# Kernel optimization log

Measured on AMD Instinct MI355X. Metric: run time of the kernel, lower is better.

The kernel has to match this reference:

```python
import jax, jax.numpy as jnp
import numpy as np

B, C, H, W = 128, 512, 14, 14
HEADS = 4
DH = C // HEADS  # 128
RH = RW = 7      # reduced KV grid (hardcoded 7x7 in source)
EPS = 1e-5
SCALE = DH ** -0.5


def _rel_pos_index():
    # replicates RelativePositionBias.__init__ index construction (h=w=7)
    coords = np.stack(np.meshgrid(np.arange(RH), np.arange(RW), indexing='ij'))
    cf = coords.reshape(2, -1)                       # [2,49]
    rc = cf[:, :, None] - cf[:, None, :]             # [2,49,49]
    rc = rc.transpose(1, 2, 0).copy()                # [49,49,2]
    rc[:, :, 0] += RH - 1
    rc[:, :, 1] += RW - 1
    rc[:, :, 0] *= 2 * RH - 1
    return rc.sum(-1)                                # [49,49] int

REL_IDX = _rel_pos_index()


def batchnorm(x, g, b, m, v):
    inv = g / jnp.sqrt(v + EPS)
    return x * inv[None, :, None, None] + (b - m * inv)[None, :, None, None]


def dsconv(x, w_dw, w_pw):
    # depthwise 3x3 (pad 1, groups=C) then pointwise 1x1, no bias
    cin = x.shape[1]
    y = jax.lax.conv_general_dilated(
        x, w_dw, window_strides=(1, 1), padding=((1, 1), (1, 1)),
        dimension_numbers=('NCHW', 'OIHW', 'NCHW'), feature_group_count=cin)
    return jnp.einsum('bchw,oc->bohw', y, w_pw)


def bilinear_to_7(x):
    # F.interpolate(size=(7,7), mode='bilinear', align_corners=True)
    hin, win = x.shape[2], x.shape[3]
    ys = jnp.linspace(0.0, hin - 1, RH)
    xs = jnp.linspace(0.0, win - 1, RW)
    y0 = jnp.floor(ys).astype(jnp.int32); y1 = jnp.minimum(y0 + 1, hin - 1)
    x0 = jnp.floor(xs).astype(jnp.int32); x1 = jnp.minimum(x0 + 1, win - 1)
    wy = (ys - y0)[:, None]                          # [7,1]
    wx = (xs - x0)[None, :]                          # [1,7]
    v00 = x[:, :, y0][:, :, :, x0]; v01 = x[:, :, y0][:, :, :, x1]
    v10 = x[:, :, y1][:, :, :, x0]; v11 = x[:, :, y1][:, :, :, x1]
    top = v00 * (1 - wx) + v01 * wx
    bot = v10 * (1 - wx) + v11 * wx
    return top * (1 - wy) + bot * wy


def _to_heads(t, h, w):
    # 'b (dim_head heads) h w -> b heads (h w) dim_head'
    b = t.shape[0]
    return jnp.transpose(t.reshape(b, DH, HEADS, h * w), (0, 2, 3, 1))


def setup_inputs() -> dict:
    key = jax.random.key(0)
    ks = jax.random.split(key, 16)
    p = {}
    p['x'] = jax.random.normal(ks[0], (B, C, H, W), jnp.float32)
    p['bn1_g'] = jax.random.normal(ks[1], (C,), jnp.float32) * 0.1 + 1.0
    p['bn1_b'] = jax.random.normal(ks[2], (C,), jnp.float32) * 0.1
    p['bn1_m'] = jax.random.normal(ks[3], (C,), jnp.float32) * 0.1
    p['bn1_v'] = jax.random.uniform(ks[4], (C,), jnp.float32, 0.5, 1.5)
    p['w_qkv_dw'] = jax.random.normal(ks[5], (C, 1, 3, 3), jnp.float32) * 0.1
    p['w_qkv_pw'] = jax.random.normal(ks[6], (3 * C, C), jnp.float32) * (C ** -0.5)
    p['rel_table'] = jax.random.normal(ks[7], ((2 * RH - 1) * (2 * RW - 1), HEADS), jnp.float32) * 0.02
    p['w_out_dw'] = jax.random.normal(ks[8], (C, 1, 3, 3), jnp.float32) * 0.1
    p['w_out_pw'] = jax.random.normal(ks[9], (C, C), jnp.float32) * (C ** -0.5)
    p['bn2_g'] = jax.random.normal(ks[10], (C,), jnp.float32) * 0.1 + 1.0
    p['bn2_b'] = jax.random.normal(ks[11], (C,), jnp.float32) * 0.1
    p['bn2_m'] = jax.random.normal(ks[12], (C,), jnp.float32) * 0.1
    p['bn2_v'] = jax.random.uniform(ks[13], (C,), jnp.float32, 0.5, 1.5)
    p['w_mlp'] = jax.random.normal(ks[14], (C, C), jnp.float32) * (C ** -0.5)
    return p


def reference(x, bn1_g, bn1_b, bn1_m, bn1_v, w_qkv_dw, w_qkv_pw, rel_table,
              w_out_dw, w_out_pw, bn2_g, bn2_b, bn2_m, bn2_v, w_mlp):
    out = batchnorm(x, bn1_g, bn1_b, bn1_m, bn1_v)
    qkv = dsconv(out, w_qkv_dw, w_qkv_pw)            # [B,3C,H,W]
    q, k, v = jnp.split(qkv, 3, axis=1)
    k = bilinear_to_7(k)
    v = bilinear_to_7(v)
    q = _to_heads(q, H, W)                           # [B,h,196,dh]
    k = _to_heads(k, RH, RW)                         # [B,h,49,dh]
    v = _to_heads(v, RH, RW)
    attn = jnp.einsum('bhid,bhjd->bhij', q, k)       # [B,h,196,49]
    # gathered relative-position bias, expanded 7x7 -> 14x14 via repeat_interleave
    bias = rel_table[REL_IDX.reshape(-1)].reshape(RH, RW, RH * RW, HEADS)
    bias = jnp.repeat(bias, 2, axis=0)
    bias = jnp.repeat(bias, 2, axis=1)               # [14,14,49,heads]
    bias = jnp.transpose(bias.reshape(H * W, RH * RW, HEADS), (2, 0, 1))[None]
    attn = (attn + bias) * SCALE                     # NOTE: scale applied after bias (faithful)
    attn = jax.nn.softmax(attn, axis=-1)
    o = jnp.einsum('bhij,bhjd->bhid', attn, v)       # [B,h,196,dh]
    o = jnp.transpose(o, (0, 3, 1, 2)).reshape(x.shape[0], C, H, W)
    o = dsconv(o, w_out_dw, w_out_pw)
    out = o + x
    residue = out
    out = batchnorm(out, bn2_g, bn2_b, bn2_m, bn2_v)
    out = jax.nn.relu(out)
    out = jnp.einsum('bchw,oc->bohw', out, w_mlp)
    return out + residue
```

## Files before the change

kernel.cpp:

```cpp
#include <hip/hip_runtime.h>

typedef short bf16x8 __attribute__((ext_vector_type(8)));
typedef float f32x4 __attribute__((ext_vector_type(4)));
typedef unsigned short u16;

#define ATT_SCALE 0.08838834764831845f

__device__ __forceinline__ u16 cvt_bf(float f) {
    union { float f; unsigned u; } a; a.f = f;
    unsigned r = a.u + 0x7FFFu + ((a.u >> 16) & 1u);
    return (u16)(r >> 16);
}

__device__ __forceinline__ void gload_lds16(const void* g, void* l) {
    __builtin_amdgcn_global_load_lds(
        (const __attribute__((address_space(1))) unsigned int*)g,
        (__attribute__((address_space(3))) unsigned int*)l, 16, 0, 0);
}

__global__ __launch_bounds__(256) void k0_prep(
    const float* __restrict__ wqkv, const float* __restrict__ wout,
    const float* __restrict__ wmlp,
    const float* __restrict__ g1, const float* __restrict__ b1,
    const float* __restrict__ m1, const float* __restrict__ v1,
    const float* __restrict__ g2, const float* __restrict__ b2,
    const float* __restrict__ m2, const float* __restrict__ v2,
    u16* __restrict__ W1p, u16* __restrict__ W2p, u16* __restrict__ W3p,
    float* __restrict__ s1, float* __restrict__ t1,
    float* __restrict__ s2, float* __restrict__ t2)
{
    int idx = blockIdx.x * 256 + threadIdx.x;
    if (idx < 786432) {
        int o = idx >> 9, c = idx & 511;
        int part = o >> 9, wi = o & 511;
        int hh = wi >> 7, dd = wi & 127;
        int orig = part * 512 + dd * 4 + hh;
        W1p[idx] = cvt_bf(wqkv[orig * 512 + c]);
    } else if (idx < 1048576) {
        int j = idx - 786432;
        int o = j >> 9, cp = j & 511;
        int oc = ((cp & 127) << 2) | (cp >> 7);
        W2p[j] = cvt_bf(wout[o * 512 + oc]);
    } else if (idx < 1310720) {
        int j = idx - 1048576;
        W3p[j] = cvt_bf(wmlp[j]);
    } else if (idx < 1311232) {
        int c = idx - 1310720;
        float i1 = g1[c] / sqrtf(v1[c] + 1e-5f);
        s1[c] = i1; t1[c] = b1[c] - m1[c] * i1;
        float i2 = g2[c] / sqrtf(v2[c] + 1e-5f);
        s2[c] = i2; t2[c] = b2[c] - m2[c] * i2;
    }
}

__global__ __launch_bounds__(256) void k1_bn_dw_bil(
    const float* __restrict__ x, const float* __restrict__ wdw,
    const float* __restrict__ s1, const float* __restrict__ t1,
    u16* __restrict__ ybf, u16* __restrict__ ybil)
{
    __shared__ float xs[32][197];
    __shared__ float ys[32][197];
    __shared__ float wt[32][9];
    __shared__ float sc[32], tc[32];
    int b = blockIdx.x >> 4, cg = blockIdx.x & 15;
    int c0 = cg * 32;
    int t = threadIdx.x;
    if (t < 32) { sc[t] = s1[c0 + t]; tc[t] = t1[c0 + t]; }
    for (int i = t; i < 288; i += 256) wt[i / 9][i % 9] = wdw[(c0 + i / 9) * 9 + i % 9];
    __syncthreads();
    const float* xb = x + ((size_t)b * 512 + c0) * 196;
    for (int i = t; i < 6272; i += 256) {
        int c = i / 196, p = i - c * 196;
        xs[c][p] = xb[i] * sc[c] + tc[c];
    }
    __syncthreads();
    for (int i = t; i < 6272; i += 256) {
        int c = i & 31, p = i >> 5;
        int ii = p / 14, jj = p - ii * 14;
        float acc = 0.f;
        #pragma unroll
        for (int di = -1; di <= 1; ++di) {
            int i2 = ii + di;
            if (i2 < 0 || i2 > 13) continue;
            #pragma unroll
            for (int dj = -1; dj <= 1; ++dj) {
                int j2 = jj + dj;
                if (j2 < 0 || j2 > 13) continue;
                acc += wt[c][(di + 1) * 3 + (dj + 1)] * xs[c][i2 * 14 + j2];
            }
        }
        ys[c][p] = acc;
        ybf[((size_t)b * 196 + p) * 512 + c0 + c] = cvt_bf(acc);
    }
    __syncthreads();
    for (int i = t; i < 1568; i += 256) {
        int c = i & 31, r = i >> 5;
        int ri = r / 7, rj = r - ri * 7;
        float fy = 13.f * ri / 6.f, fx = 13.f * rj / 6.f;
        int y0 = (int)fy; int y1 = min(y0 + 1, 13);
        int x0 = (int)fx; int x1 = min(x0 + 1, 13);
        float wy = fy - y0, wx = fx - x0;
        float v00 = ys[c][y0 * 14 + x0], v01 = ys[c][y0 * 14 + x1];
        float v10 = ys[c][y1 * 14 + x0], v11 = ys[c][y1 * 14 + x1];
        float top = v00 + (v01 - v00) * wx;
        float bot = v10 + (v11 - v10) * wx;
        float r7  = top + (bot - top) * wy;
        ybil[((size_t)b * 49 + r) * 512 + c0 + c] = cvt_bf(r7);
    }
}

template<int EPI>
__global__ __launch_bounds__(256, 2) void gemm_tn(
    const u16* __restrict__ A, const u16* __restrict__ Bw,
    float* __restrict__ out, int ldo,
    const float* __restrict__ auxf, u16* __restrict__ auxb,
    const float* __restrict__ s2, const float* __restrict__ t2)
{
    __shared__ __attribute__((aligned(16))) char smA[8192];
    __shared__ __attribute__((aligned(16))) char smB[8192];
    int t = threadIdx.x;
    int wv = t >> 6, l = t & 63;
    int wr = wv >> 1, wc = wv & 1;
    int m0 = blockIdx.x * 128, n0 = blockIdx.y * 128;
    f32x4 acc[4][4];
    #pragma unroll
    for (int mi = 0; mi < 4; ++mi)
        #pragma unroll
        for (int ni = 0; ni < 4; ++ni)
            acc[mi][ni] = f32x4{0.f, 0.f, 0.f, 0.f};

    const char* Ag = (const char*)A + (size_t)(m0 + (t >> 2)) * 1024 + ((t & 3) << 4);
    const char* Bg = (const char*)Bw + (size_t)(n0 + (t >> 2)) * 1024 + ((t & 3) << 4);
    char* lA = smA + wv * 1024;
    char* lB = smB + wv * 1024;
    int kb = (l >> 4) << 4;
    int rA = wr * 64 + (l & 15);
    int rB = wc * 64 + (l & 15);

    for (int kt = 0; kt < 16; ++kt) {
        __syncthreads();
        gload_lds16(Ag, lA);
        gload_lds16(Ag + 65536, lA + 4096);
        gload_lds16(Bg, lB);
        gload_lds16(Bg + 65536, lB + 4096);
        Ag += 64; Bg += 64;
        __syncthreads();
        bf16x8 af[4], bfr[4];
        #pragma unroll
        for (int mi = 0; mi < 4; ++mi)
            af[mi] = *(const bf16x8*)(smA + (rA + mi * 16) * 64 + kb);
        #pragma unroll
        for (int ni = 0; ni < 4; ++ni)
            bfr[ni] = *(const bf16x8*)(smB + (rB + ni * 16) * 64 + kb);
        #pragma unroll
        for (int mi = 0; mi < 4; ++mi)
            #pragma unroll
            for (int ni = 0; ni < 4; ++ni)
                acc[mi][ni] = __builtin_amdgcn_mfma_f32_16x16x32_bf16(af[mi], bfr[ni], acc[mi][ni], 0, 0, 0);
    }

    #pragma unroll
    for (int mi = 0; mi < 4; ++mi) {
        int rowg = m0 + wr * 64 + mi * 16 + ((l >> 4) << 2);
        if (EPI == 0) {
            #pragma unroll
            for (int ni = 0; ni < 4; ++ni) {
                int colg = n0 + wc * 64 + ni * 16 + (l & 15);
                float* op = out + (size_t)rowg * ldo + colg;
                #pragma unroll
                for (int v = 0; v < 4; ++v) op[(size_t)v * ldo] = acc[mi][ni][v];
            }
        } else if (EPI == 3) {
            #pragma unroll
            for (int ni = 0; ni < 4; ++ni) {
                int colg = n0 + wc * 64 + ni * 16 + (l & 15);
                #pragma unroll
                for (int v = 0; v < 4; ++v)
                    auxb[(size_t)(rowg + v) * ldo + colg] = cvt_bf(acc[mi][ni][v]);
            }
        } else if (EPI == 1) {
            int bb = rowg / 196, pp = rowg - bb * 196;
            #pragma unroll
            for (int ni = 0; ni < 4; ++ni) {
                int colg = n0 + wc * 64 + ni * 16 + (l & 15);
                float4 xv = *(const float4*)(auxf + (size_t)bb * 100352 + (size_t)colg * 196 + pp);
                const float* xa = (const float*)&xv;
                float ss = s2[colg], tt = t2[colg];
                #pragma unroll
                for (int v = 0; v < 4; ++v) {
                    float rv = acc[mi][ni][v] + xa[v];
                    out[(size_t)(rowg + v) * 512 + colg] = rv;
                    float av = rv * ss + tt;
                    av = av > 0.f ? av : 0.f;
                    auxb[(size_t)(rowg + v) * 512 + colg] = cvt_bf(av);
                }
            }
        } else {
            int bb = rowg / 196, pp = rowg - bb * 196;
            #pragma unroll
            for (int ni = 0; ni < 4; ++ni) {
                int colg = n0 + wc * 64 + ni * 16 + (l & 15);
                float4 dv;
                float* da = (float*)&dv;
                #pragma unroll
                for (int v = 0; v < 4; ++v)
                    da[v] = acc[mi][ni][v] + auxf[(size_t)(rowg + v) * 512 + colg];
                *(float4*)(out + (size_t)bb * 100352 + (size_t)colg * 196 + pp) = dv;
            }
        }
    }
}

#define K4_KLS   0
#define K4_VT    16384
#define K4_BIAS  32768
#define K4_SHR   45312
__global__ __launch_bounds__(256) void k4_attn(
    const u16* __restrict__ qbf, const u16* __restrict__ kvbf,
    const float* __restrict__ rel, float* __restrict__ O)
{
    __shared__ __attribute__((aligned(16))) char sm[61696];
    int b = blockIdx.x >> 2, h = blockIdx.x & 3;
    int t = threadIdx.x, w = t >> 6, l = t & 63;
    const char* kvbase = (const char*)(kvbf + (size_t)b * 49 * 1024 + h * 128);
    for (int id = t; id < 1024; id += 256) {
        int r = id >> 4, c = id & 15;
        uint4 kvv = make_uint4(0, 0, 0, 0), vvv = make_uint4(0, 0, 0, 0);
        if (r < 49) {
            kvv = *(const uint4*)(kvbase + (size_t)r * 2048 + c * 16);
            vvv = *(const uint4*)(kvbase + (size_t)r * 2048 + 1024 + c * 16);
        }
        *(uint4*)(sm + K4_KLS + r * 256 + ((c ^ (r & 15)) * 16)) = kvv;
        *(uint4*)(sm + K4_SHR + r * 256 + c * 16) = vvv;
    }
    float* bias7 = (float*)(sm + K4_BIAS);
    for (int id = t; id < 3136; id += 256) {
        int q7 = id >> 6, j = id & 63;
        float bv = -1e30f;
        if (j < 49) {
            int ki = j / 7, kj = j - ki * 7;
            int qi = q7 / 7, qj = q7 - qi * 7;
            bv = rel[((qi - ki + 6) * 13 + (qj - kj + 6)) * 4 + h];
        }
        bias7[id] = bv;
    }
    __syncthreads();
    for (int li = 0; li < 4; ++li) {
        int id = li * 256 + t;
        int d = id & 127, jc = id >> 7;
        u16 vals[8];
        #pragma unroll
        for (int i = 0; i < 8; ++i)
            vals[i] = *(const u16*)(sm + K4_SHR + (jc * 8 + i) * 256 + d * 2);
        *(uint4*)(sm + K4_VT + d * 128 + ((jc ^ (d & 7)) * 16)) = *(uint4*)vals;
    }
    __syncthreads();
    const u16* qb = qbf + (size_t)b * 196 * 512 + h * 128;
    float* Ob = O + (size_t)b * 196 * 512 + h * 128;
    char* Pls = sm + K4_SHR + w * 2048;
    for (int mt = w; mt < 13; mt += 4) {
        int m0 = mt * 16;
        int pa = m0 + (l & 15);
        const u16* qrow = qb + (size_t)pa * 512 + ((l >> 4) << 3);
        bf16x8 qf[4];
        #pragma unroll
        for (int kk = 0; kk < 4; ++kk) {
            bf16x8 z = {0, 0, 0, 0, 0, 0, 0, 0};
            qf[kk] = (pa < 196) ? *(const bf16x8*)(qrow + kk * 32) : z;
        }
        f32x4 s[4];
        #pragma unroll
        for (int nt = 0; nt < 4; ++nt) s[nt] = f32x4{0.f, 0.f, 0.f, 0.f};
        #pragma unroll
        for (int kk = 0; kk < 4; ++kk)
            #pragma unroll
            for (int nt = 0; nt < 4; ++nt) {
                int row = nt * 16 + (l & 15);
                bf16x8 kf = *(const bf16x8*)(sm + K4_KLS + row * 256 + (((kk * 4 + (l >> 4)) ^ (row & 15)) * 16));
                s[nt] = __builtin_amdgcn_mfma_f32_16x16x32_bf16(qf[kk], kf, s[nt], 0, 0, 0);
            }
        asm volatile("s_waitcnt lgkmcnt(0)" ::: "memory");
        float inv[4];
        #pragma unroll
        for (int v = 0; v < 4; ++v) {
            int p = m0 + ((l >> 4) << 2) + v;
            int pc = p < 196 ? p : 195;
            int ih = pc / 14, iw = pc - ih * 14;
            int q7 = (ih >> 1) * 7 + (iw >> 1);
            float sv[4];
            float mx = -3.0e38f;
            #pragma unroll
            for (int nt = 0; nt < 4; ++nt) {
                sv[nt] = (s[nt][v] + bias7[q7 * 64 + nt * 16 + (l & 15)]) * ATT_SCALE;
                mx = fmaxf(mx, sv[nt]);
            }
            #pragma unroll
            for (int o = 8; o >= 1; o >>= 1) mx = fmaxf(mx, __shfl_xor(mx, o));
            float den = 0.f, e[4];
            #pragma unroll
            for (int nt = 0; nt < 4; ++nt) { e[nt] = __expf(sv[nt] - mx); den += e[nt]; }
            #pragma unroll
            for (int o = 8; o >= 1; o >>= 1) den += __shfl_xor(den, o);
            inv[v] = 1.f / den;
            int row = ((l >> 4) << 2) + v;
            #pragma unroll
            for (int nt = 0; nt < 4; ++nt) {
                int col = nt * 16 + (l & 15);
                *(u16*)(Pls + row * 128 + (((col >> 3) ^ (row & 7)) * 16) + ((col & 7) * 2)) = cvt_bf(e[nt]);
            }
        }
        asm volatile("s_waitcnt lgkmcnt(0)" ::: "memory");
        __builtin_amdgcn_sched_barrier(0);
        f32x4 o[8];
        #pragma unroll
        for (int nt2 = 0; nt2 < 8; ++nt2) o[nt2] = f32x4{0.f, 0.f, 0.f, 0.f};
        #pragma unroll
        for (int kk = 0; kk < 2; ++kk) {
            int rowp = l & 15;
            bf16x8 pf = *(const bf16x8*)(Pls + rowp * 128 + (((kk * 4 + (l >> 4)) ^ (rowp & 7)) * 16));
            #pragma unroll
            for (int nt2 = 0; nt2 < 8; ++nt2) {
                int d = nt2 * 16 + (l & 15);
                bf16x8 vf = *(const bf16x8*)(sm + K4_VT + d * 128 + (((kk * 4 + (l >> 4)) ^ (d & 7)) * 16));
                o[nt2] = __builtin_amdgcn_mfma_f32_16x16x32_bf16(pf, vf, o[nt2], 0, 0, 0);
            }
        }
        #pragma unroll
        for (int nt2 = 0; nt2 < 8; ++nt2) {
            #pragma unroll
            for (int v = 0; v < 4; ++v) {
                int p = m0 + ((l >> 4) << 2) + v;
                if (p < 196)
                    Ob[(size_t)p * 512 + nt2 * 16 + (l & 15)] = o[nt2][v] * inv[v];
            }
        }
    }
}

__global__ __launch_bounds__(256) void k5_dw2(
    const float* __restrict__ O, const float* __restrict__ wdw,
    u16* __restrict__ z)
{
    __shared__ float xs[32][197];
    __shared__ float wt[32][9];
    int b = blockIdx.x >> 4, cg = blockIdx.x & 15;
    int c0 = cg * 32;
    int t = threadIdx.x;
    for (int i = t; i < 288; i += 256) {
        int cl = i / 9;
        int cp = c0 + cl;
        int corig = ((cp & 127) << 2) | (cp >> 7);
        wt[cl][i % 9] = wdw[corig * 9 + i % 9];
    }
    const float* Ob = O + (size_t)b * 196 * 512 + c0;
    for (int i = t; i < 6272; i += 256) {
        int c = i & 31, p = i >> 5;
        xs[c][p] = Ob[(size_t)p * 512 + c];
    }
    __syncthreads();
    for (int i = t; i < 6272; i += 256) {
        int c = i & 31, p = i >> 5;
        int ii = p / 14, jj = p - ii * 14;
        float acc = 0.f;
        #pragma unroll
        for (int di = -1; di <= 1; ++di) {
            int i2 = ii + di;
            if (i2 < 0 || i2 > 13) continue;
            #pragma unroll
            for (int dj = -1; dj <= 1; ++dj) {
                int j2 = jj + dj;
                if (j2 < 0 || j2 > 13) continue;
                acc += wt[c][(di + 1) * 3 + (dj + 1)] * xs[c][i2 * 14 + j2];
            }
        }
        z[((size_t)b * 196 + p) * 512 + c0 + c] = cvt_bf(acc);
    }
}

extern "C" void kernel_launch(void* const* d_in, const int* in_sizes, int n_in,
                              void* d_out, int out_size, void* d_ws, size_t ws_size,
                              hipStream_t stream)
{
    const float* x    = (const float*)d_in[0];
    const float* g1   = (const float*)d_in[1];
    const float* b1   = (const float*)d_in[2];
    const float* m1   = (const float*)d_in[3];
    const float* v1   = (const float*)d_in[4];
    const float* wqdw = (const float*)d_in[5];
    const float* wqpw = (const float*)d_in[6];
    const float* rel  = (const float*)d_in[7];
    const float* wodw = (const float*)d_in[8];
    const float* wopw = (const float*)d_in[9];
    const float* g2   = (const float*)d_in[10];
    const float* b2   = (const float*)d_in[11];
    const float* m2   = (const float*)d_in[12];
    const float* v2   = (const float*)d_in[13];
    const float* wmlp = (const float*)d_in[14];

    char* ws = (char*)d_ws;
    size_t off = 0;
    auto alloc = [&](size_t bytes) { char* p = ws + off; off += (bytes + 255) & ~(size_t)255; return p; };
    u16* W1p  = (u16*)alloc(1536ull * 512 * 2);
    u16* W2p  = (u16*)alloc(512ull * 512 * 2);
    u16* W3p  = (u16*)alloc(512ull * 512 * 2);
    float* s1 = (float*)alloc(512 * 4);
    float* t1 = (float*)alloc(512 * 4);
    float* s2 = (float*)alloc(512 * 4);
    float* t2 = (float*)alloc(512 * 4);
    u16* ybf  = (u16*)alloc(25088ull * 512 * 2);
    u16* ybil = (u16*)alloc(6272ull * 512 * 2);
    float* qbuf = (float*)alloc(25088ull * 512 * 4);
    float* kv7  = (float*)alloc(6272ull * 1024 * 4);
    float* Obuf = (float*)alloc(25088ull * 512 * 4);
    (void)ws_size; (void)in_sizes; (void)n_in; (void)out_size;

    u16* qbf  = (u16*)qbuf;
    u16* kvbf = (u16*)kv7;

    k0_prep<<<5122, 256, 0, stream>>>(wqpw, wopw, wmlp, g1, b1, m1, v1, g2, b2, m2, v2,
                                      W1p, W2p, W3p, s1, t1, s2, t2);
    k1_bn_dw_bil<<<2048, 256, 0, stream>>>(x, wqdw, s1, t1, ybf, ybil);
    gemm_tn<3><<<dim3(196, 4), 256, 0, stream>>>(ybf, W1p, nullptr, 512, nullptr, qbf, nullptr, nullptr);
    gemm_tn<3><<<dim3(49, 8), 256, 0, stream>>>(ybil, W1p + 262144, nullptr, 1024, nullptr, kvbf, nullptr, nullptr);
    k4_attn<<<512, 256, 0, stream>>>(qbf, kvbf, rel, Obuf);
    u16* zbuf = (u16*)kv7;
    k5_dw2<<<2048, 256, 0, stream>>>(Obuf, wodw, zbuf);
    float* resid = qbuf;
    u16* abuf = ybf;
    gemm_tn<1><<<dim3(196, 4), 256, 0, stream>>>(zbuf, W2p, resid, 512, x, abuf, s2, t2);
    gemm_tn<2><<<dim3(196, 4), 256, 0, stream>>>(abuf, W3p, (float*)d_out, 512, resid, nullptr, nullptr, nullptr);
}
```

Baseline: 376.7 us.

## Store attention output and depthwise LDS tiles in bf16, vectorize x loads

The attention kernel now writes its output in bf16 instead of fp32, which halves the write traffic of k4 and the read traffic of the second depthwise kernel. Both depthwise kernels hold their LDS tiles as bf16, with row padding changed to 199, which cuts shared memory use and may allow more resident blocks. The first kernel also reads x with float4 loads. In exchange, the normalized input, the depthwise intermediate and the attention output are rounded to bf16 one step earlier, adding some numerical error.

```diff
diff --git a/kernel.cpp b/kernel.cpp
--- a/kernel.cpp
+++ b/kernel.cpp
@@ -10,6 +10,11 @@
     union { float f; unsigned u; } a; a.f = f;
     unsigned r = a.u + 0x7FFFu + ((a.u >> 16) & 1u);
     return (u16)(r >> 16);
+}
+
+__device__ __forceinline__ float bf2f(u16 h) {
+    union { unsigned u; float f; } a; a.u = ((unsigned)h) << 16;
+    return a.f;
 }
 
 __device__ __forceinline__ void gload_lds16(const void* g, void* l) {
@@ -58,8 +63,8 @@
     const float* __restrict__ s1, const float* __restrict__ t1,
     u16* __restrict__ ybf, u16* __restrict__ ybil)
 {
-    __shared__ float xs[32][197];
-    __shared__ float ys[32][197];
+    __shared__ u16 xs[32][199];
+    __shared__ u16 ys[32][199];
     __shared__ float wt[32][9];
     __shared__ float sc[32], tc[32];
     int b = blockIdx.x >> 4, cg = blockIdx.x & 15;
@@ -68,10 +73,15 @@
     if (t < 32) { sc[t] = s1[c0 + t]; tc[t] = t1[c0 + t]; }
     for (int i = t; i < 288; i += 256) wt[i / 9][i % 9] = wdw[(c0 + i / 9) * 9 + i % 9];
     __syncthreads();
-    const float* xb = x + ((size_t)b * 512 + c0) * 196;
-    for (int i = t; i < 6272; i += 256) {
-        int c = i / 196, p = i - c * 196;
-        xs[c][p] = xb[i] * sc[c] + tc[c];
+    const float4* xb4 = (const float4*)(x + ((size_t)b * 512 + c0) * 196);
+    for (int i = t; i < 1568; i += 256) {
+        int c = i / 49, j = i - c * 49;
+        float4 v = xb4[i];
+        float ss = sc[c], tt = tc[c];
+        xs[c][4 * j]     = cvt_bf(v.x * ss + tt);
+        xs[c][4 * j + 1] = cvt_bf(v.y * ss + tt);
+        xs[c][4 * j + 2] = cvt_bf(v.z * ss + tt);
+        xs[c][4 * j + 3] = cvt_bf(v.w * ss + tt);
     }
     __syncthreads();
     for (int i = t; i < 6272; i += 256) {
@@ -86,11 +96,12 @@
             for (int dj = -1; dj <= 1; ++dj) {
                 int j2 = jj + dj;
                 if (j2 < 0 || j2 > 13) continue;
-                acc += wt[c][(di + 1) * 3 + (dj + 1)] * xs[c][i2 * 14 + j2];
-            }
-        }
-        ys[c][p] = acc;
-        ybf[((size_t)b * 196 + p) * 512 + c0 + c] = cvt_bf(acc);
+                acc += wt[c][(di + 1) * 3 + (dj + 1)] * bf2f(xs[c][i2 * 14 + j2]);
+            }
+        }
+        u16 ab = cvt_bf(acc);
+        ys[c][p] = ab;
+        ybf[((size_t)b * 196 + p) * 512 + c0 + c] = ab;
     }
     __syncthreads();
     for (int i = t; i < 1568; i += 256) {
@@ -100,8 +111,8 @@
         int y0 = (int)fy; int y1 = min(y0 + 1, 13);
         int x0 = (int)fx; int x1 = min(x0 + 1, 13);
         float wy = fy - y0, wx = fx - x0;
-        float v00 = ys[c][y0 * 14 + x0], v01 = ys[c][y0 * 14 + x1];
-        float v10 = ys[c][y1 * 14 + x0], v11 = ys[c][y1 * 14 + x1];
+        float v00 = bf2f(ys[c][y0 * 14 + x0]), v01 = bf2f(ys[c][y0 * 14 + x1]);
+        float v10 = bf2f(ys[c][y1 * 14 + x0]), v11 = bf2f(ys[c][y1 * 14 + x1]);
         float top = v00 + (v01 - v00) * wx;
         float bot = v10 + (v11 - v10) * wx;
         float r7  = top + (bot - top) * wy;
@@ -217,7 +228,7 @@
 #define K4_SHR   45312
 __global__ __launch_bounds__(256) void k4_attn(
     const u16* __restrict__ qbf, const u16* __restrict__ kvbf,
-    const float* __restrict__ rel, float* __restrict__ O)
+    const float* __restrict__ rel, u16* __restrict__ O)
 {
     __shared__ __attribute__((aligned(16))) char sm[61696];
     int b = blockIdx.x >> 2, h = blockIdx.x & 3;
@@ -256,7 +267,7 @@
     }
     __syncthreads();
     const u16* qb = qbf + (size_t)b * 196 * 512 + h * 128;
-    float* Ob = O + (size_t)b * 196 * 512 + h * 128;
+    u16* Ob = O + (size_t)b * 196 * 512 + h * 128;
     char* Pls = sm + K4_SHR + w * 2048;
     for (int mt = w; mt < 13; mt += 4) {
         int m0 = mt * 16;
@@ -331,17 +342,17 @@
             for (int v = 0; v < 4; ++v) {
                 int p = m0 + ((l >> 4) << 2) + v;
                 if (p < 196)
-                    Ob[(size_t)p * 512 + nt2 * 16 + (l & 15)] = o[nt2][v] * inv[v];
+                    Ob[(size_t)p * 512 + nt2 * 16 + (l & 15)] = cvt_bf(o[nt2][v] * inv[v]);
             }
         }
     }
 }
 
 __global__ __launch_bounds__(256) void k5_dw2(
-    const float* __restrict__ O, const float* __restrict__ wdw,
+    const u16* __restrict__ O, const float* __restrict__ wdw,
     u16* __restrict__ z)
 {
-    __shared__ float xs[32][197];
+    __shared__ u16 xs[32][199];
     __shared__ float wt[32][9];
     int b = blockIdx.x >> 4, cg = blockIdx.x & 15;
     int c0 = cg * 32;
@@ -352,7 +363,7 @@
         int corig = ((cp & 127) << 2) | (cp >> 7);
         wt[cl][i % 9] = wdw[corig * 9 + i % 9];
     }
-    const float* Ob = O + (size_t)b * 196 * 512 + c0;
+    const u16* Ob = O + (size_t)b * 196 * 512 + c0;
     for (int i = t; i < 6272; i += 256) {
         int c = i & 31, p = i >> 5;
         xs[c][p] = Ob[(size_t)p * 512 + c];
@@ -370,7 +381,7 @@
             for (int dj = -1; dj <= 1; ++dj) {
                 int j2 = jj + dj;
                 if (j2 < 0 || j2 > 13) continue;
-                acc += wt[c][(di + 1) * 3 + (dj + 1)] * xs[c][i2 * 14 + j2];
+                acc += wt[c][(di + 1) * 3 + (dj + 1)] * bf2f(xs[c][i2 * 14 + j2]);
             }
         }
         z[((size_t)b * 196 + p) * 512 + c0 + c] = cvt_bf(acc);
@@ -411,7 +422,7 @@
     u16* ybil = (u16*)alloc(6272ull * 512 * 2);
     float* qbuf = (float*)alloc(25088ull * 512 * 4);
     float* kv7  = (float*)alloc(6272ull * 1024 * 4);
-    float* Obuf = (float*)alloc(25088ull * 512 * 4);
+    u16* Obuf = (u16*)alloc(25088ull * 512 * 2);
     (void)ws_size; (void)in_sizes; (void)n_in; (void)out_size;
 
     u16* qbf  = (u16*)qbuf;
```

New measurement: 358.8 us. 1.05x faster.
